# Performance work log

Measured on AMD Instinct MI355X. Metric: run time of the kernel, lower is better.

## Reference

```python
import jax, jax.numpy as jnp
import numpy as np

N = 50000
E = 800000
IN = 128
H = 4
C = 32
HC = H * C  # 128
LN_EPS = 1e-5


def _lin(key, fan_in, fan_out):
    kw, kb = jax.random.split(key)
    w = jax.random.normal(kw, (fan_in, fan_out), jnp.float32) * (1.0 / np.sqrt(fan_in))
    b = jax.random.normal(kb, (fan_out,), jnp.float32) * 0.01
    return w, b


def setup_inputs() -> dict:
    key = jax.random.key(0)
    ks = jax.random.split(key, 16)
    x = jax.random.normal(ks[0], (N, IN), jnp.float32)
    edge_index = jax.random.randint(ks[1], (2, E), 0, N, jnp.int64)
    Wq1, bq1 = _lin(ks[2], IN, HC)
    Wk1, bk1 = _lin(ks[3], IN, HC)
    Wv1, bv1 = _lin(ks[4], IN, HC)
    Ws1, bs1 = _lin(ks[5], IN, HC)
    g1 = jnp.ones((HC,), jnp.float32)
    be1 = jnp.zeros((HC,), jnp.float32)
    Wq2, bq2 = _lin(ks[6], HC, HC)
    Wk2, bk2 = _lin(ks[7], HC, HC)
    Wv2, bv2 = _lin(ks[8], HC, HC)
    Ws2, bs2 = _lin(ks[9], HC, HC)
    g2 = jnp.ones((HC,), jnp.float32)
    be2 = jnp.zeros((HC,), jnp.float32)
    return dict(x=x, edge_index=edge_index,
                Wq1=Wq1, bq1=bq1, Wk1=Wk1, bk1=bk1, Wv1=Wv1, bv1=bv1, Ws1=Ws1, bs1=bs1,
                g1=g1, be1=be1,
                Wq2=Wq2, bq2=bq2, Wk2=Wk2, bk2=bk2, Wv2=Wv2, bv2=bv2, Ws2=Ws2, bs2=bs2,
                g2=g2, be2=be2)


def transformer_conv(x, src, dst, Wq, bq, Wk, bk, Wv, bv, Ws, bs):
    # x: [N, F_in]; src/dst: [E] (messages flow src -> dst, PyG source_to_target)
    n = x.shape[0]
    q = (x @ Wq + bq).reshape(n, H, C)
    k = (x @ Wk + bk).reshape(n, H, C)
    v = (x @ Wv + bv).reshape(n, H, C)
    # per-edge attention logits: [E, H]
    alpha = jnp.einsum('ehc,ehc->eh', q[dst], k[src]) / np.sqrt(C)
    # segment-softmax over incoming edges of each target node
    amax = jax.ops.segment_max(alpha, dst, num_segments=n)      # [N, H]
    ex = jnp.exp(alpha - amax[dst])                             # [E, H]
    denom = jax.ops.segment_sum(ex, dst, num_segments=n)        # [N, H]
    w = ex / denom[dst]                                         # [E, H]
    msg = w[:, :, None] * v[src]                                # [E, H, C]
    agg = jax.ops.segment_sum(msg, dst, num_segments=n)         # [N, H, C]
    return agg.reshape(n, HC) + x @ Ws + bs                     # root/skip connection


def layer_norm(x, g, b):
    mu = jnp.mean(x, axis=-1, keepdims=True)
    var = jnp.mean(jnp.square(x - mu), axis=-1, keepdims=True)
    return (x - mu) * jax.lax.rsqrt(var + LN_EPS) * g + b


def reference(x, edge_index,
              Wq1, bq1, Wk1, bk1, Wv1, bv1, Ws1, bs1, g1, be1,
              Wq2, bq2, Wk2, bk2, Wv2, bv2, Ws2, bs2, g2, be2):
    src, dst = edge_index[0], edge_index[1]
    h = transformer_conv(x, src, dst, Wq1, bq1, Wk1, bk1, Wv1, bv1, Ws1, bs1)
    h = jax.nn.relu(layer_norm(h, g1, be1))
    h = transformer_conv(h, src, dst, Wq2, bq2, Wk2, bk2, Wv2, bv2, Ws2, bs2)
    return layer_norm(h, g2, be2)
```

## Files before the change

kernel.cpp:

```cpp
#include <hip/hip_runtime.h>
#include <math.h>

#define LN_EPS 1e-5f
#define ATT_SCALE 0.17677669529663687f
#define MAXDEG 64

typedef __attribute__((ext_vector_type(8))) short bf16x8;
typedef __attribute__((ext_vector_type(4))) float f32x4;
typedef __attribute__((ext_vector_type(2))) _Float16 half2_t;

__device__ __forceinline__ unsigned short f2b(float f) {
    unsigned u = __float_as_uint(f);
    unsigned r = (u + 0x7FFFu + ((u >> 16) & 1)) >> 16;
    return (unsigned short)r;
}
__device__ __forceinline__ half2_t bc(unsigned u) {
    return __builtin_bit_cast(half2_t, u);
}
__device__ __forceinline__ unsigned pk(float a, float b) {
    return __builtin_bit_cast(unsigned, __builtin_amdgcn_cvt_pkrtz(a, b));
}

__global__ __launch_bounds__(256) void prep_kernel(
    const float* __restrict__ W0, const float* __restrict__ W1,
    const float* __restrict__ W2, const float* __restrict__ W3,
    const float* __restrict__ W4, const float* __restrict__ W5,
    const float* __restrict__ W6, const float* __restrict__ W7,
    unsigned short* __restrict__ wf, int* __restrict__ cursor, int n)
{
    if (blockIdx.x >= 64) {
        int i = (blockIdx.x - 64) * 256 + threadIdx.x;
        if (i < n) cursor[i] = 0;
        return;
    }
    int t = blockIdx.x * 256 + threadIdx.x;
    int mi = t >> 11, cb = (t >> 8) & 7, tk = (t >> 6) & 3, lane = t & 63;
    const float* W;
    switch (mi) {
        case 0: W = W0; break; case 1: W = W1; break;
        case 2: W = W2; break; case 3: W = W3; break;
        case 4: W = W4; break; case 5: W = W5; break;
        case 6: W = W6; break; default: W = W7; break;
    }
    int hi = lane >> 4, c = lane & 15;
    int col = cb * 16 + c;
    union { bf16x8 vec; unsigned short u[8]; } o;
    #pragma unroll
    for (int j = 0; j < 8; ++j) {
        int k = tk * 32 + hi * 8 + j;
        o.u[j] = f2b(W[k * 128 + col]);
    }
    *(bf16x8*)(wf + (size_t)t * 8) = o.vec;
}

template <bool F32IN>
__device__ __forceinline__ void proj_body(
    const void* __restrict__ xin, const unsigned short* __restrict__ wf,
    const float* __restrict__ b0, const float* __restrict__ b1,
    const float* __restrict__ b2, const float* __restrict__ b3,
    _Float16* __restrict__ qh, _Float16* __restrict__ kvh,
    _Float16* __restrict__ sph, int n, int bid)
{
    const float* biases[4] = {b0, b1, b2, b3};
    int wave = threadIdx.x >> 6, lane = threadIdx.x & 63;
    int rb0 = (bid * 4 + wave) * 2;
    int rr = lane & 15, hi = lane >> 4;

    bf16x8 af[2][4];
    #pragma unroll
    for (int rb2 = 0; rb2 < 2; ++rb2) {
        int row = (rb0 + rb2) * 16 + rr;
        #pragma unroll
        for (int t = 0; t < 4; ++t) {
            if (F32IN) {
                const float* xf = (const float*)xin;
                union { bf16x8 v; unsigned short u[8]; } o;
                if (row < n) {
                    float4 a = *(const float4*)(xf + (size_t)row * 128 + t * 32 + hi * 8);
                    float4 b = *(const float4*)(xf + (size_t)row * 128 + t * 32 + hi * 8 + 4);
                    o.u[0]=f2b(a.x); o.u[1]=f2b(a.y); o.u[2]=f2b(a.z); o.u[3]=f2b(a.w);
                    o.u[4]=f2b(b.x); o.u[5]=f2b(b.y); o.u[6]=f2b(b.z); o.u[7]=f2b(b.w);
                } else {
                    #pragma unroll
                    for (int j = 0; j < 8; ++j) o.u[j] = 0;
                }
                af[rb2][t] = o.v;
            } else {
                const unsigned short* xb = (const unsigned short*)xin;
                af[rb2][t] = *(const bf16x8*)(xb + (size_t)row * 128 + t * 32 + hi * 8);
            }
        }
    }

    int node0 = rb0 * 16 + rr;
    int node1 = node0 + 16;

    #pragma unroll
    for (int mi = 0; mi < 4; ++mi) {
        const bf16x8* wfv = (const bf16x8*)(wf + (size_t)mi * 16384);
        const float* bias = biases[mi];
        #pragma unroll
        for (int cb = 0; cb < 8; ++cb) {
            f32x4 acc0 = {0.f, 0.f, 0.f, 0.f};
            f32x4 acc1 = {0.f, 0.f, 0.f, 0.f};
            #pragma unroll
            for (int t = 0; t < 4; ++t) {
                bf16x8 wfr = wfv[(cb * 4 + t) * 64 + lane];
                acc0 = __builtin_amdgcn_mfma_f32_16x16x32_bf16(wfr, af[0][t], acc0, 0, 0, 0);
                acc1 = __builtin_amdgcn_mfma_f32_16x16x32_bf16(wfr, af[1][t], acc1, 0, 0, 0);
            }
            int m0 = cb * 16 + hi * 4;
            float4 bb = *(const float4*)&bias[m0];
            uint2 w0, w1;
            w0.x = pk(acc0[0] + bb.x, acc0[1] + bb.y);
            w0.y = pk(acc0[2] + bb.z, acc0[3] + bb.w);
            w1.x = pk(acc1[0] + bb.x, acc1[1] + bb.y);
            w1.y = pk(acc1[2] + bb.z, acc1[3] + bb.w);
            size_t o0, o1;
            _Float16* base;
            if (mi == 0)      { base = qh;  o0 = (size_t)node0 * 128 + m0;       o1 = (size_t)node1 * 128 + m0; }
            else if (mi == 1) { base = kvh; o0 = (size_t)node0 * 256 + m0;       o1 = (size_t)node1 * 256 + m0; }
            else if (mi == 2) { base = kvh; o0 = (size_t)node0 * 256 + 128 + m0; o1 = (size_t)node1 * 256 + 128 + m0; }
            else              { base = sph; o0 = (size_t)node0 * 128 + m0;       o1 = (size_t)node1 * 128 + m0; }
            if (node0 < n) *(uint2*)(base + o0) = w0;
            if (node1 < n) *(uint2*)(base + o1) = w1;
        }
    }
}

__device__ __forceinline__ void fill_body(
    const int* __restrict__ src, const int* __restrict__ dst,
    int* __restrict__ cursor, unsigned short* __restrict__ csr, int E, int fb)
{
    int t = fb * 256 + threadIdx.x;
    int e = t * 4;
    if (e + 3 < E) {
        int4 s = *(const int4*)(src + e);
        int4 d = *(const int4*)(dst + e);
        int p0 = atomicAdd(&cursor[d.x], 1);
        int p1 = atomicAdd(&cursor[d.y], 1);
        int p2 = atomicAdd(&cursor[d.z], 1);
        int p3 = atomicAdd(&cursor[d.w], 1);
        if (p0 < MAXDEG) csr[d.x * MAXDEG + p0] = (unsigned short)s.x;
        if (p1 < MAXDEG) csr[d.y * MAXDEG + p1] = (unsigned short)s.y;
        if (p2 < MAXDEG) csr[d.z * MAXDEG + p2] = (unsigned short)s.z;
        if (p3 < MAXDEG) csr[d.w * MAXDEG + p3] = (unsigned short)s.w;
    } else {
        for (int i = e; i < E; ++i) {
            int d = dst[i];
            int p = atomicAdd(&cursor[d], 1);
            if (p < MAXDEG) csr[d * MAXDEG + p] = (unsigned short)src[i];
        }
    }
}

__global__ __launch_bounds__(256) void fused_l1_kernel(
    const float* __restrict__ x, const unsigned short* __restrict__ wf,
    const float* __restrict__ b0, const float* __restrict__ b1,
    const float* __restrict__ b2, const float* __restrict__ b3,
    _Float16* __restrict__ qh, _Float16* __restrict__ kvh,
    _Float16* __restrict__ sph, int n, int nblk,
    const int* __restrict__ src, const int* __restrict__ dst,
    int* __restrict__ cursor, unsigned short* __restrict__ csr, int E)
{
    if ((int)blockIdx.x < nblk)
        proj_body<true>(x, wf, b0, b1, b2, b3, qh, kvh, sph, n, blockIdx.x);
    else
        fill_body(src, dst, cursor, csr, E, blockIdx.x - nblk);
}

__global__ __launch_bounds__(256) void proj_mfma_kernel(
    const unsigned short* __restrict__ xb, const unsigned short* __restrict__ wf,
    const float* __restrict__ b0, const float* __restrict__ b1,
    const float* __restrict__ b2, const float* __restrict__ b3,
    _Float16* __restrict__ qh, _Float16* __restrict__ kvh,
    _Float16* __restrict__ sph, int n)
{
    proj_body<false>(xb, wf, b0, b1, b2, b3, qh, kvh, sph, n, blockIdx.x);
}

__global__ __launch_bounds__(256) void attn_ln_kernel(
    const uint4* __restrict__ qh4,
    const uint4* __restrict__ kv4,
    const uint4* __restrict__ sph4,
    const int* __restrict__ cursor,
    const unsigned short* __restrict__ csr,
    const float4* __restrict__ g4, const float4* __restrict__ b4,
    float4* __restrict__ outf, uint4* __restrict__ outb,
    int n, int relu)
{
    int node = blockIdx.x * 4 + (threadIdx.x >> 6);
    if (node >= n) return;
    int lane = threadIdx.x & 63;
    int slot = lane >> 4, ll = lane & 15;

    uint4 qw = qh4[(size_t)node * 16 + ll];

    int cnt = cursor[node];
    int e0 = node * MAXDEG, e1 = e0 + cnt;
    int T = (cnt + 3) >> 2;

    float m = -1e30f, ss = 0.f;
    float a[8];
    #pragma unroll
    for (int j = 0; j < 8; ++j) a[j] = 0.f;

    int idx = e0 + slot;
    int vA = (idx < e1);
    int sA = vA ? ((int)csr[idx] << 5) : 0;
    uint4 kA = kv4[(size_t)sA + ll];
    uint4 vA4 = kv4[(size_t)sA + 16 + ll];

    for (int t = 0; t < T; ++t) {
        int nidx = idx + 4;
        int vN = (nidx < e1);
        int sN = vN ? ((int)csr[nidx] << 5) : 0;
        uint4 kN = kv4[(size_t)sN + ll];
        uint4 vN4 = kv4[(size_t)sN + 16 + ll];

        float dot = 0.f;
        dot = __builtin_amdgcn_fdot2(bc(kA.x), bc(qw.x), dot, false);
        dot = __builtin_amdgcn_fdot2(bc(kA.y), bc(qw.y), dot, false);
        dot = __builtin_amdgcn_fdot2(bc(kA.z), bc(qw.z), dot, false);
        dot = __builtin_amdgcn_fdot2(bc(kA.w), bc(qw.w), dot, false);
        dot += __shfl_xor(dot, 1);
        dot += __shfl_xor(dot, 2);

        float al = vA ? dot * ATT_SCALE : -1e38f;
        float d = al - m;
        if (__any(d > 20.f)) {
            float mn = fmaxf(m, al);
            float c = __expf(m - mn);
            ss *= c;
            #pragma unroll
            for (int j = 0; j < 8; ++j) a[j] *= c;
            m = mn;
            d = al - m;
        }
        float w = __expf(d);
        ss += w;
        half2_t p0 = bc(vA4.x), p1 = bc(vA4.y), p2 = bc(vA4.z), p3 = bc(vA4.w);
        a[0] = fmaf(w, (float)p0[0], a[0]); a[1] = fmaf(w, (float)p0[1], a[1]);
        a[2] = fmaf(w, (float)p1[0], a[2]); a[3] = fmaf(w, (float)p1[1], a[3]);
        a[4] = fmaf(w, (float)p2[0], a[4]); a[5] = fmaf(w, (float)p2[1], a[5]);
        a[6] = fmaf(w, (float)p3[0], a[6]); a[7] = fmaf(w, (float)p3[1], a[7]);

        idx = nidx; vA = vN; kA = kN; vA4 = vN4;
    }

    float mg = m;
    mg = fmaxf(mg, __shfl_xor(mg, 16));
    mg = fmaxf(mg, __shfl_xor(mg, 32));
    float sc = __expf(m - mg);
    float ssg = ss * sc;
    ssg += __shfl_xor(ssg, 16);
    ssg += __shfl_xor(ssg, 32);
    #pragma unroll
    for (int j = 0; j < 8; ++j) {
        float aj = a[j] * sc;
        aj += __shfl_xor(aj, 16);
        aj += __shfl_xor(aj, 32);
        a[j] = aj;
    }

    float inv = (ssg > 0.f) ? 1.f / ssg : 0.f;
    uint4 sw = sph4[(size_t)node * 16 + ll];
    half2_t s0 = bc(sw.x), s1 = bc(sw.y), s2 = bc(sw.z), s3 = bc(sw.w);
    float o[8];
    o[0]=fmaf(a[0],inv,(float)s0[0]); o[1]=fmaf(a[1],inv,(float)s0[1]);
    o[2]=fmaf(a[2],inv,(float)s1[0]); o[3]=fmaf(a[3],inv,(float)s1[1]);
    o[4]=fmaf(a[4],inv,(float)s2[0]); o[5]=fmaf(a[5],inv,(float)s2[1]);
    o[6]=fmaf(a[6],inv,(float)s3[0]); o[7]=fmaf(a[7],inv,(float)s3[1]);

    float sum = o[0]+o[1]+o[2]+o[3]+o[4]+o[5]+o[6]+o[7];
    sum += __shfl_xor(sum, 1); sum += __shfl_xor(sum, 2);
    sum += __shfl_xor(sum, 4); sum += __shfl_xor(sum, 8);
    float mu = sum * (1.f / 128.f);
    float var = 0.f;
    float d8[8];
    #pragma unroll
    for (int j = 0; j < 8; ++j) { d8[j] = o[j] - mu; var = fmaf(d8[j], d8[j], var); }
    var += __shfl_xor(var, 1); var += __shfl_xor(var, 2);
    var += __shfl_xor(var, 4); var += __shfl_xor(var, 8);
    float rstd = rsqrtf(var * (1.f / 128.f) + LN_EPS);

    float4 gg0 = g4[2 * ll], gg1 = g4[2 * ll + 1];
    float4 bb0 = b4[2 * ll], bb1 = b4[2 * ll + 1];
    float r[8];
    r[0]=fmaf(d8[0]*rstd, gg0.x, bb0.x); r[1]=fmaf(d8[1]*rstd, gg0.y, bb0.y);
    r[2]=fmaf(d8[2]*rstd, gg0.z, bb0.z); r[3]=fmaf(d8[3]*rstd, gg0.w, bb0.w);
    r[4]=fmaf(d8[4]*rstd, gg1.x, bb1.x); r[5]=fmaf(d8[5]*rstd, gg1.y, bb1.y);
    r[6]=fmaf(d8[6]*rstd, gg1.z, bb1.z); r[7]=fmaf(d8[7]*rstd, gg1.w, bb1.w);

    if (slot == 0) {
        if (relu) {
            #pragma unroll
            for (int j = 0; j < 8; ++j) r[j] = fmaxf(r[j], 0.f);
            uint4 ow;
            ow.x = (unsigned)f2b(r[0]) | ((unsigned)f2b(r[1]) << 16);
            ow.y = (unsigned)f2b(r[2]) | ((unsigned)f2b(r[3]) << 16);
            ow.z = (unsigned)f2b(r[4]) | ((unsigned)f2b(r[5]) << 16);
            ow.w = (unsigned)f2b(r[6]) | ((unsigned)f2b(r[7]) << 16);
            outb[(size_t)node * 16 + ll] = ow;
        } else {
            outf[(size_t)node * 32 + 2 * ll]     = make_float4(r[0], r[1], r[2], r[3]);
            outf[(size_t)node * 32 + 2 * ll + 1] = make_float4(r[4], r[5], r[6], r[7]);
        }
    }
}

extern "C" void kernel_launch(void* const* d_in, const int* in_sizes, int n_in,
                              void* d_out, int out_size, void* d_ws, size_t ws_size,
                              hipStream_t stream) {
    const float* x  = (const float*)d_in[0];
    const int*   ei = (const int*)d_in[1];
    const int n = in_sizes[0] / 128;
    const int E = in_sizes[1] / 2;
    const int* src = ei;
    const int* dst = ei + E;

    const float *Wq1 = (const float*)d_in[2],  *bq1 = (const float*)d_in[3];
    const float *Wk1 = (const float*)d_in[4],  *bk1 = (const float*)d_in[5];
    const float *Wv1 = (const float*)d_in[6],  *bv1 = (const float*)d_in[7];
    const float *Ws1 = (const float*)d_in[8],  *bs1 = (const float*)d_in[9];
    const float *g1  = (const float*)d_in[10], *be1 = (const float*)d_in[11];
    const float *Wq2 = (const float*)d_in[12], *bq2 = (const float*)d_in[13];
    const float *Wk2 = (const float*)d_in[14], *bk2 = (const float*)d_in[15];
    const float *Wv2 = (const float*)d_in[16], *bv2 = (const float*)d_in[17];
    const float *Ws2 = (const float*)d_in[18], *bs2 = (const float*)d_in[19];
    const float *g2  = (const float*)d_in[20], *be2 = (const float*)d_in[21];

    const int nrb     = (n + 15) / 16;
    const int nblk    = (nrb + 7) / 8;
    const int padrows = nblk * 8 * 16;

    const size_t nf = (size_t)n * 128;
    char* w = (char*)d_ws;
    _Float16* qh  = (_Float16*)w; w += nf * sizeof(_Float16);
    _Float16* sph = (_Float16*)w; w += nf * sizeof(_Float16);
    _Float16* kvh = (_Float16*)w; w += (size_t)n * 256 * sizeof(_Float16);
    unsigned short* hb = (unsigned short*)w; w += (size_t)padrows * 128 * sizeof(unsigned short);
    unsigned short* wf = (unsigned short*)w; w += (size_t)8 * 16384 * sizeof(unsigned short);
    int* cursor  = (int*)w; w += (size_t)(n + 1) * sizeof(int);
    unsigned short* csr = (unsigned short*)w; w += (size_t)n * MAXDEG * sizeof(unsigned short);

    int prepBlocks = 64 + (n + 255) / 256;
    int fillBlocks = (E / 4 + 255) / 256 + 1;
    int nodeBlocks = (n + 3) / 4;

    prep_kernel<<<prepBlocks, 256, 0, stream>>>(Wq1, Wk1, Wv1, Ws1,
                                                Wq2, Wk2, Wv2, Ws2, wf, cursor, n);

    fused_l1_kernel<<<nblk + fillBlocks, 256, 0, stream>>>(
        x, wf, bq1, bk1, bv1, bs1, qh, kvh, sph, n, nblk,
        src, dst, cursor, csr, E);

    attn_ln_kernel<<<nodeBlocks, 256, 0, stream>>>((const uint4*)qh, (const uint4*)kvh,
                                                   (const uint4*)sph, cursor, csr,
                                                   (const float4*)g1, (const float4*)be1,
                                                   nullptr, (uint4*)hb, n, 1);

    proj_mfma_kernel<<<nblk, 256, 0, stream>>>(hb, wf + (size_t)4 * 16384,
                                               bq2, bk2, bv2, bs2,
                                               qh, kvh, sph, n);
    attn_ln_kernel<<<nodeBlocks, 256, 0, stream>>>((const uint4*)qh, (const uint4*)kvh,
                                                   (const uint4*)sph, cursor, csr,
                                                   (const float4*)g2, (const float4*)be2,
                                                   (float4*)d_out, nullptr, n, 0);
}
```

Before: 230.4 us.

## Fuse layer-1 attention+LayerNorm with layer-2 projection via shared-memory tile

Layer-1 attention, LayerNorm and ReLU now run in a 1024-thread block of 16 nodes that writes the hidden rows to LDS as fp16. Four waves of the same block then do the layer-2 QKV/skip projection with f16 MFMA. This drops the bf16 hidden-state round trip through global memory and one kernel launch, with the layer-2 weights switched to fp16 to match. The edge-fill portion now handles 8 edges per thread and is ordered before the projection blocks. The cost is an idle barrier for 12 of the 16 waves during the projection phase and larger blocks that may lower occupancy.

```diff
diff --git a/kernel.cpp b/kernel.cpp
--- a/kernel.cpp
+++ b/kernel.cpp
@@ -6,6 +6,7 @@
 #define MAXDEG 64
 
 typedef __attribute__((ext_vector_type(8))) short bf16x8;
+typedef __attribute__((ext_vector_type(8))) _Float16 f16x8;
 typedef __attribute__((ext_vector_type(4))) float f32x4;
 typedef __attribute__((ext_vector_type(2))) _Float16 half2_t;
 
@@ -48,14 +49,15 @@
     #pragma unroll
     for (int j = 0; j < 8; ++j) {
         int k = tk * 32 + hi * 8 + j;
-        o.u[j] = f2b(W[k * 128 + col]);
+        float v = W[k * 128 + col];
+        o.u[j] = (mi < 4) ? f2b(v)
+                          : __builtin_bit_cast(unsigned short, (_Float16)v);
     }
     *(bf16x8*)(wf + (size_t)t * 8) = o.vec;
 }
 
-template <bool F32IN>
-__device__ __forceinline__ void proj_body(
-    const void* __restrict__ xin, const unsigned short* __restrict__ wf,
+__device__ __forceinline__ void proj_body_l1(
+    const float* __restrict__ xf, const unsigned short* __restrict__ wf,
     const float* __restrict__ b0, const float* __restrict__ b1,
     const float* __restrict__ b2, const float* __restrict__ b3,
     _Float16* __restrict__ qh, _Float16* __restrict__ kvh,
@@ -72,23 +74,17 @@
         int row = (rb0 + rb2) * 16 + rr;
         #pragma unroll
         for (int t = 0; t < 4; ++t) {
-            if (F32IN) {
-                const float* xf = (const float*)xin;
-                union { bf16x8 v; unsigned short u[8]; } o;
-                if (row < n) {
-                    float4 a = *(const float4*)(xf + (size_t)row * 128 + t * 32 + hi * 8);
-                    float4 b = *(const float4*)(xf + (size_t)row * 128 + t * 32 + hi * 8 + 4);
-                    o.u[0]=f2b(a.x); o.u[1]=f2b(a.y); o.u[2]=f2b(a.z); o.u[3]=f2b(a.w);
-                    o.u[4]=f2b(b.x); o.u[5]=f2b(b.y); o.u[6]=f2b(b.z); o.u[7]=f2b(b.w);
-                } else {
-                    #pragma unroll
-                    for (int j = 0; j < 8; ++j) o.u[j] = 0;
-                }
-                af[rb2][t] = o.v;
+            union { bf16x8 v; unsigned short u[8]; } o;
+            if (row < n) {
+                float4 a = *(const float4*)(xf + (size_t)row * 128 + t * 32 + hi * 8);
+                float4 b = *(const float4*)(xf + (size_t)row * 128 + t * 32 + hi * 8 + 4);
+                o.u[0]=f2b(a.x); o.u[1]=f2b(a.y); o.u[2]=f2b(a.z); o.u[3]=f2b(a.w);
+                o.u[4]=f2b(b.x); o.u[5]=f2b(b.y); o.u[6]=f2b(b.z); o.u[7]=f2b(b.w);
             } else {
-                const unsigned short* xb = (const unsigned short*)xin;
-                af[rb2][t] = *(const bf16x8*)(xb + (size_t)row * 128 + t * 32 + hi * 8);
+                #pragma unroll
+                for (int j = 0; j < 8; ++j) o.u[j] = 0;
             }
+            af[rb2][t] = o.v;
         }
     }
 
@@ -133,18 +129,28 @@
     int* __restrict__ cursor, unsigned short* __restrict__ csr, int E, int fb)
 {
     int t = fb * 256 + threadIdx.x;
-    int e = t * 4;
-    if (e + 3 < E) {
-        int4 s = *(const int4*)(src + e);
-        int4 d = *(const int4*)(dst + e);
-        int p0 = atomicAdd(&cursor[d.x], 1);
-        int p1 = atomicAdd(&cursor[d.y], 1);
-        int p2 = atomicAdd(&cursor[d.z], 1);
-        int p3 = atomicAdd(&cursor[d.w], 1);
-        if (p0 < MAXDEG) csr[d.x * MAXDEG + p0] = (unsigned short)s.x;
-        if (p1 < MAXDEG) csr[d.y * MAXDEG + p1] = (unsigned short)s.y;
-        if (p2 < MAXDEG) csr[d.z * MAXDEG + p2] = (unsigned short)s.z;
-        if (p3 < MAXDEG) csr[d.w * MAXDEG + p3] = (unsigned short)s.w;
+    int e = t * 8;
+    if (e + 7 < E) {
+        int4 s0 = *(const int4*)(src + e);
+        int4 s1 = *(const int4*)(src + e + 4);
+        int4 d0 = *(const int4*)(dst + e);
+        int4 d1 = *(const int4*)(dst + e + 4);
+        int p0 = atomicAdd(&cursor[d0.x], 1);
+        int p1 = atomicAdd(&cursor[d0.y], 1);
+        int p2 = atomicAdd(&cursor[d0.z], 1);
+        int p3 = atomicAdd(&cursor[d0.w], 1);
+        int p4 = atomicAdd(&cursor[d1.x], 1);
+        int p5 = atomicAdd(&cursor[d1.y], 1);
+        int p6 = atomicAdd(&cursor[d1.z], 1);
+        int p7 = atomicAdd(&cursor[d1.w], 1);
+        if (p0 < MAXDEG) csr[d0.x * MAXDEG + p0] = (unsigned short)s0.x;
+        if (p1 < MAXDEG) csr[d0.y * MAXDEG + p1] = (unsigned short)s0.y;
+        if (p2 < MAXDEG) csr[d0.z * MAXDEG + p2] = (unsigned short)s0.z;
+        if (p3 < MAXDEG) csr[d0.w * MAXDEG + p3] = (unsigned short)s0.w;
+        if (p4 < MAXDEG) csr[d1.x * MAXDEG + p4] = (unsigned short)s1.x;
+        if (p5 < MAXDEG) csr[d1.y * MAXDEG + p5] = (unsigned short)s1.y;
+        if (p6 < MAXDEG) csr[d1.z * MAXDEG + p6] = (unsigned short)s1.z;
+        if (p7 < MAXDEG) csr[d1.w * MAXDEG + p7] = (unsigned short)s1.w;
     } else {
         for (int i = e; i < E; ++i) {
             int d = dst[i];
@@ -159,35 +165,183 @@
     const float* __restrict__ b0, const float* __restrict__ b1,
     const float* __restrict__ b2, const float* __restrict__ b3,
     _Float16* __restrict__ qh, _Float16* __restrict__ kvh,
-    _Float16* __restrict__ sph, int n, int nblk,
+    _Float16* __restrict__ sph, int n, int fillBlocks,
     const int* __restrict__ src, const int* __restrict__ dst,
     int* __restrict__ cursor, unsigned short* __restrict__ csr, int E)
 {
-    if ((int)blockIdx.x < nblk)
-        proj_body<true>(x, wf, b0, b1, b2, b3, qh, kvh, sph, n, blockIdx.x);
+    if ((int)blockIdx.x < fillBlocks)
+        fill_body(src, dst, cursor, csr, E, blockIdx.x);
     else
-        fill_body(src, dst, cursor, csr, E, blockIdx.x - nblk);
-}
-
-__global__ __launch_bounds__(256) void proj_mfma_kernel(
-    const unsigned short* __restrict__ xb, const unsigned short* __restrict__ wf,
-    const float* __restrict__ b0, const float* __restrict__ b1,
-    const float* __restrict__ b2, const float* __restrict__ b3,
-    _Float16* __restrict__ qh, _Float16* __restrict__ kvh,
-    _Float16* __restrict__ sph, int n)
+        proj_body_l1(x, wf, b0, b1, b2, b3, qh, kvh, sph, n, blockIdx.x - fillBlocks);
+}
+
+__global__ __launch_bounds__(1024) void attn1_proj2_kernel(
+    const uint4* __restrict__ qh4, const uint4* __restrict__ kv4,
+    const uint4* __restrict__ sph4,
+    const int* __restrict__ cursor, const unsigned short* __restrict__ csr,
+    const float4* __restrict__ g4, const float4* __restrict__ b4,
+    const unsigned short* __restrict__ wf2,
+    const float* __restrict__ c0, const float* __restrict__ c1,
+    const float* __restrict__ c2, const float* __restrict__ c3,
+    _Float16* __restrict__ qB, _Float16* __restrict__ kvB,
+    _Float16* __restrict__ spB, int n)
 {
-    proj_body<false>(xb, wf, b0, b1, b2, b3, qh, kvh, sph, n, blockIdx.x);
+    __shared__ _Float16 hls[16][136];
+    int wv = threadIdx.x >> 6;
+    int node = blockIdx.x * 16 + wv;
+    int lane = threadIdx.x & 63;
+    int slot = lane >> 4, ll = lane & 15;
+    bool active = node < n;
+
+    float r[8];
+    if (active) {
+        uint4 qw = qh4[(size_t)node * 16 + ll];
+        int cnt = cursor[node];
+        int e0 = node * MAXDEG, e1 = e0 + cnt;
+        int T = (cnt + 3) >> 2;
+
+        float m = -1e30f, ss = 0.f;
+        float a[8];
+        #pragma unroll
+        for (int j = 0; j < 8; ++j) a[j] = 0.f;
+
+        int idx = e0 + slot;
+        int vA = (idx < e1);
+        int sA = vA ? ((int)csr[idx] << 5) : 0;
+        uint4 kA = kv4[(size_t)sA + ll];
+        uint4 vA4 = kv4[(size_t)sA + 16 + ll];
+
+        for (int t = 0; t < T; ++t) {
+            int nidx = idx + 4;
+            int vN = (nidx < e1);
+            int sN = vN ? ((int)csr[nidx] << 5) : 0;
+            uint4 kN = kv4[(size_t)sN + ll];
+            uint4 vN4 = kv4[(size_t)sN + 16 + ll];
+
+            float dot = 0.f;
+            dot = __builtin_amdgcn_fdot2(bc(kA.x), bc(qw.x), dot, false);
+            dot = __builtin_amdgcn_fdot2(bc(kA.y), bc(qw.y), dot, false);
+            dot = __builtin_amdgcn_fdot2(bc(kA.z), bc(qw.z), dot, false);
+            dot = __builtin_amdgcn_fdot2(bc(kA.w), bc(qw.w), dot, false);
+            dot += __shfl_xor(dot, 1);
+            dot += __shfl_xor(dot, 2);
+
+            float al = vA ? dot * ATT_SCALE : -1e38f;
+            float d = al - m;
+            if (__any(d > 20.f)) {
+                float mn = fmaxf(m, al);
+                float c = __expf(m - mn);
+                ss *= c;
+                #pragma unroll
+                for (int j = 0; j < 8; ++j) a[j] *= c;
+                m = mn;
+                d = al - m;
+            }
+            float w = __expf(d);
+            ss += w;
+            half2_t p0 = bc(vA4.x), p1 = bc(vA4.y), p2 = bc(vA4.z), p3 = bc(vA4.w);
+            a[0] = fmaf(w, (float)p0[0], a[0]); a[1] = fmaf(w, (float)p0[1], a[1]);
+            a[2] = fmaf(w, (float)p1[0], a[2]); a[3] = fmaf(w, (float)p1[1], a[3]);
+            a[4] = fmaf(w, (float)p2[0], a[4]); a[5] = fmaf(w, (float)p2[1], a[5]);
+            a[6] = fmaf(w, (float)p3[0], a[6]); a[7] = fmaf(w, (float)p3[1], a[7]);
+
+            idx = nidx; vA = vN; kA = kN; vA4 = vN4;
+        }
+
+        float mg = m;
+        mg = fmaxf(mg, __shfl_xor(mg, 16));
+        mg = fmaxf(mg, __shfl_xor(mg, 32));
+        float sc = __expf(m - mg);
+        float ssg = ss * sc;
+        ssg += __shfl_xor(ssg, 16);
+        ssg += __shfl_xor(ssg, 32);
+        #pragma unroll
+        for (int j = 0; j < 8; ++j) {
+            float aj = a[j] * sc;
+            aj += __shfl_xor(aj, 16);
+            aj += __shfl_xor(aj, 32);
+            a[j] = aj;
+        }
+
+        float inv = (ssg > 0.f) ? 1.f / ssg : 0.f;
+        uint4 sw = sph4[(size_t)node * 16 + ll];
+        half2_t s0 = bc(sw.x), s1 = bc(sw.y), s2 = bc(sw.z), s3 = bc(sw.w);
+        float o[8];
+        o[0]=fmaf(a[0],inv,(float)s0[0]); o[1]=fmaf(a[1],inv,(float)s0[1]);
+        o[2]=fmaf(a[2],inv,(float)s1[0]); o[3]=fmaf(a[3],inv,(float)s1[1]);
+        o[4]=fmaf(a[4],inv,(float)s2[0]); o[5]=fmaf(a[5],inv,(float)s2[1]);
+        o[6]=fmaf(a[6],inv,(float)s3[0]); o[7]=fmaf(a[7],inv,(float)s3[1]);
+
+        float sum = o[0]+o[1]+o[2]+o[3]+o[4]+o[5]+o[6]+o[7];
+        sum += __shfl_xor(sum, 1); sum += __shfl_xor(sum, 2);
+        sum += __shfl_xor(sum, 4); sum += __shfl_xor(sum, 8);
+        float mu = sum * (1.f / 128.f);
+        float var = 0.f;
+        float d8[8];
+        #pragma unroll
+        for (int j = 0; j < 8; ++j) { d8[j] = o[j] - mu; var = fmaf(d8[j], d8[j], var); }
+        var += __shfl_xor(var, 1); var += __shfl_xor(var, 2);
+        var += __shfl_xor(var, 4); var += __shfl_xor(var, 8);
+        float rstd = rsqrtf(var * (1.f / 128.f) + LN_EPS);
+
+        float4 gg0 = g4[2 * ll], gg1 = g4[2 * ll + 1];
+        float4 bb0 = b4[2 * ll], bb1 = b4[2 * ll + 1];
+        r[0]=fmaf(d8[0]*rstd, gg0.x, bb0.x); r[1]=fmaf(d8[1]*rstd, gg0.y, bb0.y);
+        r[2]=fmaf(d8[2]*rstd, gg0.z, bb0.z); r[3]=fmaf(d8[3]*rstd, gg0.w, bb0.w);
+        r[4]=fmaf(d8[4]*rstd, gg1.x, bb1.x); r[5]=fmaf(d8[5]*rstd, gg1.y, bb1.y);
+        r[6]=fmaf(d8[6]*rstd, gg1.z, bb1.z); r[7]=fmaf(d8[7]*rstd, gg1.w, bb1.w);
+    }
+
+    if (slot == 0) {
+        union { f16x8 v; uint4 u4; } hw;
+        #pragma unroll
+        for (int j = 0; j < 8; ++j)
+            hw.v[j] = active ? (_Float16)fmaxf(r[j], 0.f) : (_Float16)0.f;
+        *(uint4*)&hls[wv][ll * 8] = hw.u4;
+    }
+    __syncthreads();
+
+    if (wv < 4) {
+        int mi = wv;
+        int rr = lane & 15, hi = lane >> 4;
+        f16x8 hf[4];
+        #pragma unroll
+        for (int t = 0; t < 4; ++t)
+            hf[t] = *(const f16x8*)&hls[rr][t * 32 + hi * 8];
+        const f16x8* wfv = (const f16x8*)(wf2 + (size_t)mi * 16384);
+        const float* bias = (mi == 0) ? c0 : (mi == 1) ? c1 : (mi == 2) ? c2 : c3;
+        int node0 = blockIdx.x * 16 + rr;
+        #pragma unroll
+        for (int cb = 0; cb < 8; ++cb) {
+            f32x4 acc = {0.f, 0.f, 0.f, 0.f};
+            #pragma unroll
+            for (int t = 0; t < 4; ++t)
+                acc = __builtin_amdgcn_mfma_f32_16x16x32_f16(wfv[(cb * 4 + t) * 64 + lane],
+                                                             hf[t], acc, 0, 0, 0);
+            int m0 = cb * 16 + hi * 4;
+            float4 bb = *(const float4*)&bias[m0];
+            uint2 w0;
+            w0.x = pk(acc[0] + bb.x, acc[1] + bb.y);
+            w0.y = pk(acc[2] + bb.z, acc[3] + bb.w);
+            if (node0 < n) {
+                size_t o0;
+                _Float16* base;
+                if (mi == 0)      { base = qB;  o0 = (size_t)node0 * 128 + m0; }
+                else if (mi == 1) { base = kvB; o0 = (size_t)node0 * 256 + m0; }
+                else if (mi == 2) { base = kvB; o0 = (size_t)node0 * 256 + 128 + m0; }
+                else              { base = spB; o0 = (size_t)node0 * 128 + m0; }
+                *(uint2*)(base + o0) = w0;
+            }
+        }
+    }
 }
 
 __global__ __launch_bounds__(256) void attn_ln_kernel(
-    const uint4* __restrict__ qh4,
-    const uint4* __restrict__ kv4,
+    const uint4* __restrict__ qh4, const uint4* __restrict__ kv4,
     const uint4* __restrict__ sph4,
-    const int* __restrict__ cursor,
-    const unsigned short* __restrict__ csr,
+    const int* __restrict__ cursor, const unsigned short* __restrict__ csr,
     const float4* __restrict__ g4, const float4* __restrict__ b4,
-    float4* __restrict__ outf, uint4* __restrict__ outb,
-    int n, int relu)
+    float4* __restrict__ outf, int n)
 {
     int node = blockIdx.x * 4 + (threadIdx.x >> 6);
     if (node >= n) return;
@@ -195,7 +349,6 @@
     int slot = lane >> 4, ll = lane & 15;
 
     uint4 qw = qh4[(size_t)node * 16 + ll];
-
     int cnt = cursor[node];
     int e0 = node * MAXDEG, e1 = e0 + cnt;
     int T = (cnt + 3) >> 2;
@@ -293,19 +446,8 @@
     r[6]=fmaf(d8[6]*rstd, gg1.z, bb1.z); r[7]=fmaf(d8[7]*rstd, gg1.w, bb1.w);
 
     if (slot == 0) {
-        if (relu) {
-            #pragma unroll
-            for (int j = 0; j < 8; ++j) r[j] = fmaxf(r[j], 0.f);
-            uint4 ow;
-            ow.x = (unsigned)f2b(r[0]) | ((unsigned)f2b(r[1]) << 16);
-            ow.y = (unsigned)f2b(r[2]) | ((unsigned)f2b(r[3]) << 16);
-            ow.z = (unsigned)f2b(r[4]) | ((unsigned)f2b(r[5]) << 16);
-            ow.w = (unsigned)f2b(r[6]) | ((unsigned)f2b(r[7]) << 16);
-            outb[(size_t)node * 16 + ll] = ow;
-        } else {
-            outf[(size_t)node * 32 + 2 * ll]     = make_float4(r[0], r[1], r[2], r[3]);
-            outf[(size_t)node * 32 + 2 * ll + 1] = make_float4(r[4], r[5], r[6], r[7]);
-        }
+        outf[(size_t)node * 32 + 2 * ll]     = make_float4(r[0], r[1], r[2], r[3]);
+        outf[(size_t)node * 32 + 2 * ll + 1] = make_float4(r[4], r[5], r[6], r[7]);
     }
 }
 
@@ -330,41 +472,41 @@
     const float *Ws2 = (const float*)d_in[18], *bs2 = (const float*)d_in[19];
     const float *g2  = (const float*)d_in[20], *be2 = (const float*)d_in[21];
 
-    const int nrb     = (n + 15) / 16;
-    const int nblk    = (nrb + 7) / 8;
-    const int padrows = nblk * 8 * 16;
+    const int nrb  = (n + 15) / 16;
+    const int nblk = (nrb + 7) / 8;
+    const int fillBlocks = (E / 8 + 255) / 256 + 1;
 
     const size_t nf = (size_t)n * 128;
     char* w = (char*)d_ws;
-    _Float16* qh  = (_Float16*)w; w += nf * sizeof(_Float16);
-    _Float16* sph = (_Float16*)w; w += nf * sizeof(_Float16);
-    _Float16* kvh = (_Float16*)w; w += (size_t)n * 256 * sizeof(_Float16);
-    unsigned short* hb = (unsigned short*)w; w += (size_t)padrows * 128 * sizeof(unsigned short);
+    _Float16* qA  = (_Float16*)w; w += nf * sizeof(_Float16);
+    _Float16* spA = (_Float16*)w; w += nf * sizeof(_Float16);
+    _Float16* kvA = (_Float16*)w; w += (size_t)n * 256 * sizeof(_Float16);
+    _Float16* qB  = (_Float16*)w; w += nf * sizeof(_Float16);
+    _Float16* spB = (_Float16*)w; w += nf * sizeof(_Float16);
+    _Float16* kvB = (_Float16*)w; w += (size_t)n * 256 * sizeof(_Float16);
     unsigned short* wf = (unsigned short*)w; w += (size_t)8 * 16384 * sizeof(unsigned short);
-    int* cursor  = (int*)w; w += (size_t)(n + 1) * sizeof(int);
+    int* cursor = (int*)w; w += (size_t)(n + 1) * sizeof(int);
     unsigned short* csr = (unsigned short*)w; w += (size_t)n * MAXDEG * sizeof(unsigned short);
 
     int prepBlocks = 64 + (n + 255) / 256;
-    int fillBlocks = (E / 4 + 255) / 256 + 1;
-    int nodeBlocks = (n + 3) / 4;
+    int nodeBlocks16 = (n + 15) / 16;
+    int nodeBlocks4  = (n + 3) / 4;
 
     prep_kernel<<<prepBlocks, 256, 0, stream>>>(Wq1, Wk1, Wv1, Ws1,
                                                 Wq2, Wk2, Wv2, Ws2, wf, cursor, n);
 
-    fused_l1_kernel<<<nblk + fillBlocks, 256, 0, stream>>>(
-        x, wf, bq1, bk1, bv1, bs1, qh, kvh, sph, n, nblk,
+    fused_l1_kernel<<<fillBlocks + nblk, 256, 0, stream>>>(
+        x, wf, bq1, bk1, bv1, bs1, qA, kvA, spA, n, fillBlocks,
         src, dst, cursor, csr, E);
 
-    attn_ln_kernel<<<nodeBlocks, 256, 0, stream>>>((const uint4*)qh, (const uint4*)kvh,
-                                                   (const uint4*)sph, cursor, csr,
-                                                   (const float4*)g1, (const float4*)be1,
-                                                   nullptr, (uint4*)hb, n, 1);
-
-    proj_mfma_kernel<<<nblk, 256, 0, stream>>>(hb, wf + (size_t)4 * 16384,
-                                               bq2, bk2, bv2, bs2,
-                                               qh, kvh, sph, n);
-    attn_ln_kernel<<<nodeBlocks, 256, 0, stream>>>((const uint4*)qh, (const uint4*)kvh,
-                                                   (const uint4*)sph, cursor, csr,
-                                                   (const float4*)g2, (const float4*)be2,
-                                                   (float4*)d_out, nullptr, n, 0);
-}
+    attn1_proj2_kernel<<<nodeBlocks16, 1024, 0, stream>>>(
+        (const uint4*)qA, (const uint4*)kvA, (const uint4*)spA,
+        cursor, csr, (const float4*)g1, (const float4*)be1,
+        wf + (size_t)4 * 16384, bq2, bk2, bv2, bs2,
+        qB, kvB, spB, n);
+
+    attn_ln_kernel<<<nodeBlocks4, 256, 0, stream>>>(
+        (const uint4*)qB, (const uint4*)kvB, (const uint4*)spB,
+        cursor, csr, (const float4*)g2, (const float4*)be2,
+        (float4*)d_out, n);
+}
```

New measurement: 236.4 us. 2.6% more time.
